# Performance work log

Measured on AMD Instinct MI355X. Metric: run time of the kernel, lower is better.

The kernel has to match this reference:

```python
import jax, jax.numpy as jnp
import numpy as np
import math

N, M, K = 384, 32, 32  # x1 is (1, N, M, K)
DIM = 1                # init arg; scaled_qk = qk.div(1/sqrt(dim)) == qk * sqrt(dim)
DROP_P = 0.1


def setup_inputs() -> dict:
    key = jax.random.key(0)
    k1, k2 = jax.random.split(key)
    x1 = jax.random.normal(k1, (1, N, M, K), dtype=jnp.float32)
    # Deterministic dropout keep-mask, pre-scaled by 1/(1-p) (inverted dropout).
    u = jax.random.uniform(k2, (N, N, M, M), dtype=jnp.float32)
    dropout_mask = (u >= DROP_P).astype(jnp.float32) / (1.0 - DROP_P)
    return {"x1": x1, "dropout_mask": dropout_mask}


def reference(x1, dropout_mask):
    scale = math.sqrt(DIM)  # div by (1/sqrt(dim))
    query = x1                                   # (1, N, M, K)
    key_t = jnp.transpose(x1, (1, 0, 2, 3))      # (N, 1, M, K)
    # qk: broadcast batched matmul -> (N, N, M, M)
    qk = jnp.matmul(query, jnp.swapaxes(key_t, -2, -1))
    attn = jax.nn.softmax(qk * scale, axis=-1)   # (N, N, M, M)
    dropped = attn * dropout_mask                # dropout (training=True)
    # value = x1 (1, N, M, K) broadcasts -> output (N, N, M, K)
    out = jnp.matmul(dropped, x1)
    return out
```

## Files before the change

kernel.cpp:

```cpp
#include <hip/hip_runtime.h>
#include <hip/hip_bf16.h>

#define NN 384
#define MM 32
#define KK 32

typedef __attribute__((ext_vector_type(8))) __bf16 bf16x8;
typedef __attribute__((ext_vector_type(4))) __bf16 bf16x4;
typedef __attribute__((ext_vector_type(4))) float f32x4;

__device__ __forceinline__ void split8(const float* v, bf16x8& hi, bf16x8& lo) {
#pragma unroll
    for (int t = 0; t < 8; ++t) {
        float f = v[t];
        __bf16 h = (__bf16)f;
        hi[t] = h;
        lo[t] = (__bf16)(f - (float)h);
    }
}

__device__ __forceinline__ void split4(const float* v, bf16x4& hi, bf16x4& lo) {
#pragma unroll
    for (int t = 0; t < 4; ++t) {
        float f = v[t];
        __bf16 h = (__bf16)f;
        hi[t] = h;
        lo[t] = (__bf16)(f - (float)h);
    }
}

__global__ __launch_bounds__(256) void attn_pair_kernel(
    const float* __restrict__ x1,
    const float* __restrict__ mask,
    float* __restrict__ out)
{
    __shared__ __align__(16) __bf16 sPhi[4][32 * 40];
    __shared__ __align__(16) __bf16 sPlo[4][32 * 40];

    const int tid  = threadIdx.x;
    const int w    = tid >> 6;
    const int l    = tid & 63;
    const int m16  = l & 15;
    const int quad = l >> 4;

    const unsigned p = blockIdx.x * 4u + (unsigned)w;
    const unsigned i = p / NN;
    const unsigned j = p - i * NN;

    const float* Q  = x1 + (size_t)j * (MM * KK);
    const float* Kt = x1 + (size_t)i * (MM * KK);

    const float* mbase = mask + (size_t)p * (MM * MM);
    f32x4 mk[2][2];
#pragma unroll
    for (int aa = 0; aa < 2; ++aa)
#pragma unroll
        for (int bb = 0; bb < 2; ++bb)
            mk[aa][bb] = *(const f32x4*)(mbase + (aa * 16 + m16) * MM + bb * 16 + quad * 4);

    bf16x8 aQh[2], aQl[2], bKh[2], bKl[2];
#pragma unroll
    for (int h = 0; h < 2; ++h) {
        const int row = h * 16 + m16;
        float qbuf[8], kbuf[8];
        *(float4*)&qbuf[0] = *(const float4*)(Q  + row * KK + quad * 8);
        *(float4*)&qbuf[4] = *(const float4*)(Q  + row * KK + quad * 8 + 4);
        *(float4*)&kbuf[0] = *(const float4*)(Kt + row * KK + quad * 8);
        *(float4*)&kbuf[4] = *(const float4*)(Kt + row * KK + quad * 8 + 4);
        split8(qbuf, aQh[h], aQl[h]);
        split8(kbuf, bKh[h], bKl[h]);
    }

    f32x4 ST[2][2];
#pragma unroll
    for (int bb = 0; bb < 2; ++bb)
#pragma unroll
        for (int aa = 0; aa < 2; ++aa) {
            f32x4 c = {0.f, 0.f, 0.f, 0.f};
            c = __builtin_amdgcn_mfma_f32_16x16x32_bf16(bKl[bb], aQh[aa], c, 0, 0, 0);
            c = __builtin_amdgcn_mfma_f32_16x16x32_bf16(bKh[bb], aQl[aa], c, 0, 0, 0);
            c = __builtin_amdgcn_mfma_f32_16x16x32_bf16(bKh[bb], aQh[aa], c, 0, 0, 0);
            ST[bb][aa] = c;
        }

    float pv[2][2][4];
#pragma unroll
    for (int aa = 0; aa < 2; ++aa) {
        float mx = ST[0][aa][0];
#pragma unroll
        for (int bb = 0; bb < 2; ++bb)
#pragma unroll
            for (int r = 0; r < 4; ++r) mx = fmaxf(mx, ST[bb][aa][r]);
        mx = fmaxf(mx, __shfl_xor(mx, 16, 64));
        mx = fmaxf(mx, __shfl_xor(mx, 32, 64));

        float sum = 0.f;
#pragma unroll
        for (int bb = 0; bb < 2; ++bb)
#pragma unroll
            for (int r = 0; r < 4; ++r) {
                float e = __expf(ST[bb][aa][r] - mx);
                pv[aa][bb][r] = e;
                sum += e;
            }
        sum += __shfl_xor(sum, 16, 64);
        sum += __shfl_xor(sum, 32, 64);
        const float rinv = 1.0f / sum;
#pragma unroll
        for (int bb = 0; bb < 2; ++bb)
#pragma unroll
            for (int r = 0; r < 4; ++r)
                pv[aa][bb][r] *= rinv * mk[aa][bb][r];
    }

#pragma unroll
    for (int aa = 0; aa < 2; ++aa)
#pragma unroll
        for (int bb = 0; bb < 2; ++bb) {
            bf16x4 h4, l4;
            split4(pv[aa][bb], h4, l4);
            const int off = (aa * 16 + m16) * 40 + bb * 16 + quad * 4;
            *(bf16x4*)&sPhi[w][off] = h4;
            *(bf16x4*)&sPlo[w][off] = l4;
        }

    float vbuf[2][8];
#pragma unroll
    for (int h = 0; h < 2; ++h) {
        const float* vp = Q + (quad * 8) * KK + (h * 16 + m16);
#pragma unroll
        for (int jj = 0; jj < 8; ++jj) vbuf[h][jj] = vp[jj * KK];
    }

    asm volatile("s_waitcnt lgkmcnt(0)" ::: "memory");

    bf16x8 aPh[2], aPl[2], bVh[2], bVl[2];
#pragma unroll
    for (int h = 0; h < 2; ++h) {
        aPh[h] = *(const bf16x8*)&sPhi[w][(h * 16 + m16) * 40 + quad * 8];
        aPl[h] = *(const bf16x8*)&sPlo[w][(h * 16 + m16) * 40 + quad * 8];
        split8(vbuf[h], bVh[h], bVl[h]);
    }

    f32x4 O[2][2];
#pragma unroll
    for (int ma = 0; ma < 2; ++ma)
#pragma unroll
        for (int nk = 0; nk < 2; ++nk) {
            f32x4 c = {0.f, 0.f, 0.f, 0.f};
            c = __builtin_amdgcn_mfma_f32_16x16x32_bf16(aPl[ma], bVh[nk], c, 0, 0, 0);
            c = __builtin_amdgcn_mfma_f32_16x16x32_bf16(aPh[ma], bVl[nk], c, 0, 0, 0);
            c = __builtin_amdgcn_mfma_f32_16x16x32_bf16(aPh[ma], bVh[nk], c, 0, 0, 0);
            O[ma][nk] = c;
        }

    float* obase = out + (size_t)p * (MM * KK);
#pragma unroll
    for (int ma = 0; ma < 2; ++ma)
#pragma unroll
        for (int nk = 0; nk < 2; ++nk) {
            const int col = nk * 16 + m16;
            const int r0  = ma * 16 + quad * 4;
#pragma unroll
            for (int rr = 0; rr < 4; ++rr)
                obase[(r0 + rr) * KK + col] = O[ma][nk][rr];
        }
}

extern "C" void kernel_launch(void* const* d_in, const int* in_sizes, int n_in,
                              void* d_out, int out_size, void* d_ws, size_t ws_size,
                              hipStream_t stream) {
    const float* x1   = (const float*)d_in[0];
    const float* mask = (const float*)d_in[1];
    float* out = (float*)d_out;
    const int pairs = NN * NN;
    dim3 grid(pairs / 4), block(256);
    attn_pair_kernel<<<grid, block, 0, stream>>>(x1, mask, out);
}
```

Baseline: 1.055 ms.

## Pre-split x1 into bf16 hi/lo and transposed copies; drop LDS round-trip for P

Adds a prepass kernel that splits x1 into bf16 hi/lo parts, plus transposed copies, in the workspace. The main kernel then loads pre-split operands instead of converting fp32 in every wave. It also builds the P operand for the second MFMA directly from registers instead of staging it through shared memory, which relies on the accumulator layout matching the A-operand layout through a K-permutation that V shares. This costs an extra launch and a workspace dependency, with an fp32 fallback path when the workspace is too small.

```diff
diff --git a/kernel.cpp b/kernel.cpp
--- a/kernel.cpp
+++ b/kernel.cpp
@@ -4,6 +4,7 @@
 #define NN 384
 #define MM 32
 #define KK 32
+#define TILE (MM * KK)
 
 typedef __attribute__((ext_vector_type(8))) __bf16 bf16x8;
 typedef __attribute__((ext_vector_type(4))) __bf16 bf16x4;
@@ -19,24 +20,45 @@
     }
 }
 
-__device__ __forceinline__ void split4(const float* v, bf16x4& hi, bf16x4& lo) {
+__global__ __launch_bounds__(256) void presplit_kernel(
+    const float* __restrict__ x1,
+    __bf16* __restrict__ xhi,  __bf16* __restrict__ xlo,
+    __bf16* __restrict__ xthi, __bf16* __restrict__ xtlo)
+{
+    const int g  = blockIdx.x * 256 + threadIdx.x;
+    const int e0 = g * 4;
+    const int tile   = e0 >> 10;
+    const int within = e0 & 1023;
+    const int r  = within >> 5;
+    const int c0 = within & 31;
+
+    float4 v = *(const float4*)(x1 + e0);
+    float f[4] = {v.x, v.y, v.z, v.w};
+    bf16x4 h4, l4;
 #pragma unroll
     for (int t = 0; t < 4; ++t) {
-        float f = v[t];
-        __bf16 h = (__bf16)f;
-        hi[t] = h;
-        lo[t] = (__bf16)(f - (float)h);
-    }
-}
-
+        __bf16 h = (__bf16)f[t];
+        h4[t] = h;
+        l4[t] = (__bf16)(f[t] - (float)h);
+    }
+    *(bf16x4*)(xhi + e0) = h4;
+    *(bf16x4*)(xlo + e0) = l4;
+#pragma unroll
+    for (int t = 0; t < 4; ++t) {
+        const int to = tile * TILE + (c0 + t) * MM + r;
+        xthi[to] = h4[t];
+        xtlo[to] = l4[t];
+    }
+}
+
+template<bool PRESPLIT>
 __global__ __launch_bounds__(256) void attn_pair_kernel(
     const float* __restrict__ x1,
+    const __bf16* __restrict__ xhi,  const __bf16* __restrict__ xlo,
+    const __bf16* __restrict__ xthi, const __bf16* __restrict__ xtlo,
     const float* __restrict__ mask,
     float* __restrict__ out)
 {
-    __shared__ __align__(16) __bf16 sPhi[4][32 * 40];
-    __shared__ __align__(16) __bf16 sPlo[4][32 * 40];
-
     const int tid  = threadIdx.x;
     const int w    = tid >> 6;
     const int l    = tid & 63;
@@ -47,9 +69,6 @@
     const unsigned i = p / NN;
     const unsigned j = p - i * NN;
 
-    const float* Q  = x1 + (size_t)j * (MM * KK);
-    const float* Kt = x1 + (size_t)i * (MM * KK);
-
     const float* mbase = mask + (size_t)p * (MM * MM);
     f32x4 mk[2][2];
 #pragma unroll
@@ -59,16 +78,33 @@
             mk[aa][bb] = *(const f32x4*)(mbase + (aa * 16 + m16) * MM + bb * 16 + quad * 4);
 
     bf16x8 aQh[2], aQl[2], bKh[2], bKl[2];
-#pragma unroll
-    for (int h = 0; h < 2; ++h) {
-        const int row = h * 16 + m16;
-        float qbuf[8], kbuf[8];
-        *(float4*)&qbuf[0] = *(const float4*)(Q  + row * KK + quad * 8);
-        *(float4*)&qbuf[4] = *(const float4*)(Q  + row * KK + quad * 8 + 4);
-        *(float4*)&kbuf[0] = *(const float4*)(Kt + row * KK + quad * 8);
-        *(float4*)&kbuf[4] = *(const float4*)(Kt + row * KK + quad * 8 + 4);
-        split8(qbuf, aQh[h], aQl[h]);
-        split8(kbuf, bKh[h], bKl[h]);
+    if constexpr (PRESPLIT) {
+        const __bf16* Qh = xhi + (size_t)j * TILE;
+        const __bf16* Ql = xlo + (size_t)j * TILE;
+        const __bf16* Kh = xhi + (size_t)i * TILE;
+        const __bf16* Kl = xlo + (size_t)i * TILE;
+#pragma unroll
+        for (int h = 0; h < 2; ++h) {
+            const int off = (h * 16 + m16) * KK + quad * 8;
+            aQh[h] = *(const bf16x8*)(Qh + off);
+            aQl[h] = *(const bf16x8*)(Ql + off);
+            bKh[h] = *(const bf16x8*)(Kh + off);
+            bKl[h] = *(const bf16x8*)(Kl + off);
+        }
+    } else {
+        const float* Q  = x1 + (size_t)j * TILE;
+        const float* Kt = x1 + (size_t)i * TILE;
+#pragma unroll
+        for (int h = 0; h < 2; ++h) {
+            const int row = h * 16 + m16;
+            float qbuf[8], kbuf[8];
+            *(float4*)&qbuf[0] = *(const float4*)(Q  + row * KK + quad * 8);
+            *(float4*)&qbuf[4] = *(const float4*)(Q  + row * KK + quad * 8 + 4);
+            *(float4*)&kbuf[0] = *(const float4*)(Kt + row * KK + quad * 8);
+            *(float4*)&kbuf[4] = *(const float4*)(Kt + row * KK + quad * 8 + 4);
+            split8(qbuf, aQh[h], aQl[h]);
+            split8(kbuf, bKh[h], bKl[h]);
+        }
     }
 
     f32x4 ST[2][2];
@@ -113,33 +149,47 @@
                 pv[aa][bb][r] *= rinv * mk[aa][bb][r];
     }
 
-#pragma unroll
-    for (int aa = 0; aa < 2; ++aa)
-#pragma unroll
-        for (int bb = 0; bb < 2; ++bb) {
-            bf16x4 h4, l4;
-            split4(pv[aa][bb], h4, l4);
-            const int off = (aa * 16 + m16) * 40 + bb * 16 + quad * 4;
-            *(bf16x4*)&sPhi[w][off] = h4;
-            *(bf16x4*)&sPlo[w][off] = l4;
-        }
-
-    float vbuf[2][8];
-#pragma unroll
-    for (int h = 0; h < 2; ++h) {
-        const float* vp = Q + (quad * 8) * KK + (h * 16 + m16);
-#pragma unroll
-        for (int jj = 0; jj < 8; ++jj) vbuf[h][jj] = vp[jj * KK];
-    }
-
-    asm volatile("s_waitcnt lgkmcnt(0)" ::: "memory");
-
-    bf16x8 aPh[2], aPl[2], bVh[2], bVl[2];
-#pragma unroll
-    for (int h = 0; h < 2; ++h) {
-        aPh[h] = *(const bf16x8*)&sPhi[w][(h * 16 + m16) * 40 + quad * 8];
-        aPl[h] = *(const bf16x8*)&sPlo[w][(h * 16 + m16) * 40 + quad * 8];
-        split8(vbuf[h], bVh[h], bVl[h]);
+    bf16x8 aPh[2], aPl[2];
+#pragma unroll
+    for (int ma = 0; ma < 2; ++ma) {
+        float tmp[8];
+#pragma unroll
+        for (int r = 0; r < 4; ++r) { tmp[r] = pv[ma][0][r]; tmp[4 + r] = pv[ma][1][r]; }
+        split8(tmp, aPh[ma], aPl[ma]);
+    }
+
+    bf16x8 bVh[2], bVl[2];
+    if constexpr (PRESPLIT) {
+        const __bf16* Th = xthi + (size_t)j * TILE;
+        const __bf16* Tl = xtlo + (size_t)j * TILE;
+#pragma unroll
+        for (int nk = 0; nk < 2; ++nk) {
+            const int base = (nk * 16 + m16) * MM + quad * 4;
+            bf16x4 h0 = *(const bf16x4*)(Th + base);
+            bf16x4 h1 = *(const bf16x4*)(Th + base + 16);
+            bf16x4 l0 = *(const bf16x4*)(Tl + base);
+            bf16x4 l1 = *(const bf16x4*)(Tl + base + 16);
+            bf16x8 hv, lv;
+#pragma unroll
+            for (int t = 0; t < 4; ++t) {
+                hv[t] = h0[t]; hv[4 + t] = h1[t];
+                lv[t] = l0[t]; lv[4 + t] = l1[t];
+            }
+            bVh[nk] = hv; bVl[nk] = lv;
+        }
+    } else {
+        const float* V = x1 + (size_t)j * TILE;
+#pragma unroll
+        for (int nk = 0; nk < 2; ++nk) {
+            const int col = nk * 16 + m16;
+            float vbuf[8];
+#pragma unroll
+            for (int jj = 0; jj < 4; ++jj) {
+                vbuf[jj]     = V[(quad * 4 + jj) * KK + col];
+                vbuf[4 + jj] = V[(16 + quad * 4 + jj) * KK + col];
+            }
+            split8(vbuf, bVh[nk], bVl[nk]);
+        }
     }
 
     f32x4 O[2][2];
@@ -175,5 +225,17 @@
     float* out = (float*)d_out;
     const int pairs = NN * NN;
     dim3 grid(pairs / 4), block(256);
-    attn_pair_kernel<<<grid, block, 0, stream>>>(x1, mask, out);
-}
+
+    const size_t elems = (size_t)NN * TILE;
+    const size_t need  = elems * 2 * 4;
+    if (d_ws != nullptr && ws_size >= need) {
+        __bf16* xhi  = (__bf16*)d_ws;
+        __bf16* xlo  = xhi  + elems;
+        __bf16* xthi = xlo  + elems;
+        __bf16* xtlo = xthi + elems;
+        presplit_kernel<<<dim3(elems / 4 / 256), block, 0, stream>>>(x1, xhi, xlo, xthi, xtlo);
+        attn_pair_kernel<true><<<grid, block, 0, stream>>>(x1, xhi, xlo, xthi, xtlo, mask, out);
+    } else {
+        attn_pair_kernel<false><<<grid, block, 0, stream>>>(x1, nullptr, nullptr, nullptr, nullptr, mask, out);
+    }
+}
```

Result: faster. 1.017 ms (-3.6%).
